# Optimization experiments

Measured on AMD Instinct MI355X. Metric: run time of the kernel, lower is better.

Reference implementation:

```python
import jax, jax.numpy as jnp
import numpy as np

B, L, E, H = 2, 2048, 2048, 16
HD = E // H  # 128
ROPE_BASE = 10000.0


def setup_inputs() -> dict:
    key = jax.random.key(0)
    k1, k2, k3 = jax.random.split(key, 3)
    x = jax.random.normal(k1, (B, L, E), dtype=jnp.float32)
    position_ids = jnp.tile(jnp.arange(L, dtype=jnp.int32)[None, :], (B, 1))
    # Linear weights stored as [in, out] so y = x @ W + b (equals torch x @ W.T + b)
    W_attn = jax.random.normal(k2, (E, 3 * E), dtype=jnp.float32) * (1.0 / np.sqrt(E))
    b_attn = jnp.zeros((3 * E,), dtype=jnp.float32)
    W_proj = jax.random.normal(k3, (E, E), dtype=jnp.float32) * (1.0 / np.sqrt(E))
    b_proj = jnp.zeros((E,), dtype=jnp.float32)
    return {"x": x, "position_ids": position_ids, "W_attn": W_attn,
            "b_attn": b_attn, "W_proj": W_proj, "b_proj": b_proj}


def _rotate_half(t):
    h = t.shape[-1] // 2
    return jnp.concatenate([-t[..., h:], t[..., :h]], axis=-1)


def _apply_rope(q, k, position_ids):
    # q,k: [B,H,L,HD]; position_ids: [B,L]
    inv_freq = 1.0 / (ROPE_BASE ** (jnp.arange(0, HD, 2, dtype=jnp.float32) / HD))
    angles = position_ids.astype(jnp.float32)[:, :, None] * inv_freq  # [B,L,HD/2]
    cos = jnp.concatenate([jnp.cos(angles)] * 2, axis=-1)[:, None]  # [B,1,L,HD]
    sin = jnp.concatenate([jnp.sin(angles)] * 2, axis=-1)[:, None]
    return q * cos + _rotate_half(q) * sin, k * cos + _rotate_half(k) * sin


def reference(x, position_ids, W_attn, b_attn, W_proj, b_proj):
    # fused QKV projection
    qkv = x @ W_attn + b_attn                       # [B,L,3E]
    q, k, v = jnp.split(qkv, 3, axis=-1)            # each [B,L,E]
    reshape = lambda t: t.reshape(B, L, H, HD).transpose(0, 2, 1, 3)  # [B,H,L,HD]
    q, k, v = reshape(q), reshape(k), reshape(v)
    q, k = _apply_rope(q, k, position_ids)
    # scaled dot-product attention (mask=None -> full attention, dropout 0)
    scores = jnp.einsum('bhqd,bhkd->bhqk', q, k) * (1.0 / np.sqrt(HD))
    probs = jax.nn.softmax(scores, axis=-1)
    y = jnp.einsum('bhqk,bhkd->bhqd', probs, v)     # [B,H,L,HD]
    y = y.transpose(0, 2, 1, 3).reshape(B, L, E)
    return y @ W_proj + b_proj
```

## Files before the change

### kernel.cpp

```cpp
#include <hip/hip_runtime.h>
#include <math.h>

#define BB 2
#define LL 2048
#define EE 2048
#define HH 16
#define HD 128
#define N3E (3*EE)

typedef __attribute__((ext_vector_type(8))) short  bf16x8;
typedef __attribute__((ext_vector_type(4))) float  f32x4;

__device__ __forceinline__ ushort f2bf(float f) {
    union { float f; unsigned u; } v; v.f = f;
    unsigned u = v.u + 0x7FFFu + ((v.u >> 16) & 1u);
    return (ushort)(u >> 16);
}
__device__ __forceinline__ float bf2f(ushort u) {
    union { unsigned u; float f; } v; v.u = ((unsigned)u) << 16;
    return v.f;
}

__global__ __launch_bounds__(256) void cvt_bf16(const float* __restrict__ in,
                                                ushort* __restrict__ out, int n) {
    int i = (blockIdx.x * 256 + threadIdx.x) * 8;
    float4 a = *(const float4*)(in + i);
    float4 b = *(const float4*)(in + i + 4);
    ushort4 p0 = { f2bf(a.x), f2bf(a.y), f2bf(a.z), f2bf(a.w) };
    ushort4 p1 = { f2bf(b.x), f2bf(b.y), f2bf(b.z), f2bf(b.w) };
    *(ushort4*)(out + i)     = p0;
    *(ushort4*)(out + i + 4) = p1;
}

__global__ __launch_bounds__(256) void transpose_bf16(const float* __restrict__ in,
                                                      ushort* __restrict__ out,
                                                      int R, int Ccol) {
    __shared__ float tile[32][33];
    int c0 = blockIdx.x * 32, r0 = blockIdx.y * 32;
    int t = threadIdx.x;
    int lr = t >> 5, lc = t & 31;
    #pragma unroll
    for (int i = 0; i < 4; ++i)
        tile[lr + i * 8][lc] = in[(size_t)(r0 + lr + i * 8) * Ccol + c0 + lc];
    __syncthreads();
    #pragma unroll
    for (int i = 0; i < 4; ++i)
        out[(size_t)(c0 + lr + i * 8) * R + r0 + lc] = f2bf(tile[lc][lr + i * 8]);
}

template<int WRITE_BF16>
__global__ __launch_bounds__(256) void gemm_bt_bf16(const ushort* __restrict__ A,
                                                    const ushort* __restrict__ Bt,
                                                    const float* __restrict__ bias,
                                                    void* __restrict__ C,
                                                    int M, int N, int K) {
    __shared__ __align__(16) ushort As[128 * 32];
    __shared__ __align__(16) ushort Bs[128 * 32];
    const int t    = threadIdx.x;
    const int lane = t & 63, w = t >> 6;
    const int m    = lane & 15, quad = lane >> 4;
    const int wm   = w >> 1, wn = w & 1;
    const int m0   = blockIdx.y * 128, n0 = blockIdx.x * 128;

    f32x4 acc[4][4];
    #pragma unroll
    for (int i = 0; i < 4; ++i)
        #pragma unroll
        for (int j = 0; j < 4; ++j) acc[i][j] = (f32x4){0.f, 0.f, 0.f, 0.f};

    for (int k0 = 0; k0 < K; k0 += 32) {
        __syncthreads();
        #pragma unroll
        for (int i = 0; i < 2; ++i) {
            int c = t + i * 256;
            int row = c >> 2, kc = c & 3;
            __builtin_amdgcn_global_load_lds(
                (const __attribute__((address_space(1))) unsigned int*)(A + (size_t)(m0 + row) * K + k0 + kc * 8),
                (__attribute__((address_space(3))) unsigned int*)(As + c * 8),
                16, 0, 0);
        }
        #pragma unroll
        for (int i = 0; i < 2; ++i) {
            int c = t + i * 256;
            int row = c >> 2, kc = c & 3;
            __builtin_amdgcn_global_load_lds(
                (const __attribute__((address_space(1))) unsigned int*)(Bt + (size_t)(n0 + row) * K + k0 + kc * 8),
                (__attribute__((address_space(3))) unsigned int*)(Bs + c * 8),
                16, 0, 0);
        }
        __syncthreads();
        bf16x8 af[4], bfr[4];
        #pragma unroll
        for (int mt = 0; mt < 4; ++mt)
            af[mt] = *(const bf16x8*)&As[(wm * 64 + mt * 16 + m) * 32 + quad * 8];
        #pragma unroll
        for (int nt = 0; nt < 4; ++nt)
            bfr[nt] = *(const bf16x8*)&Bs[(wn * 64 + nt * 16 + m) * 32 + quad * 8];
        #pragma unroll
        for (int mt = 0; mt < 4; ++mt)
            #pragma unroll
            for (int nt = 0; nt < 4; ++nt)
                acc[mt][nt] = __builtin_amdgcn_mfma_f32_16x16x32_bf16(af[mt], bfr[nt], acc[mt][nt], 0, 0, 0);
    }
    #pragma unroll
    for (int mt = 0; mt < 4; ++mt) {
        #pragma unroll
        for (int nt = 0; nt < 4; ++nt) {
            #pragma unroll
            for (int r = 0; r < 4; ++r) {
                int row = m0 + wm * 64 + mt * 16 + quad * 4 + r;
                int col = n0 + wn * 64 + nt * 16 + m;
                float v = acc[mt][nt][r] + bias[col];
                if (WRITE_BF16) ((ushort*)C)[(size_t)row * N + col] = f2bf(v);
                else            ((float*)C)[(size_t)row * N + col] = v;
            }
        }
    }
}

__global__ __launch_bounds__(256) void rope_bf16(ushort* __restrict__ qkv,
                                                 const int* __restrict__ pos_ids) {
    const float scale = 0.08838834764831845f;
    int idx = blockIdx.x * 256 + threadIdx.x;
    int j  = idx & 63;
    int h  = (idx >> 6) & 15;
    int bl = idx >> 10;
    float pos = (float)pos_ids[bl];
    float inv = powf(10000.0f, -(float)(2 * j) / 128.0f);
    float ang = pos * inv;
    float s, c;
    sincosf(ang, &s, &c);
    size_t base = (size_t)bl * N3E + h * HD;
    float x1 = bf2f(qkv[base + j]), x2 = bf2f(qkv[base + j + 64]);
    qkv[base + j]      = f2bf((x1 * c - x2 * s) * scale);
    qkv[base + j + 64] = f2bf((x2 * c + x1 * s) * scale);
    base += EE;
    x1 = bf2f(qkv[base + j]); x2 = bf2f(qkv[base + j + 64]);
    qkv[base + j]      = f2bf(x1 * c - x2 * s);
    qkv[base + j + 64] = f2bf(x2 * c + x1 * s);
}

#define BQ 64
#define BKV 64
#define QKSTR 136
#define VTSTR 72

__global__ __launch_bounds__(256) void flash_mfma(const ushort* __restrict__ qkv,
                                                  ushort* __restrict__ y) {
    __shared__ __align__(16) ushort smem[22528];
    ushort* VtU = smem;
    ushort* QsU = smem;
    ushort* KsU = smem + 9216;
    ushort* PsU = smem + 9216 + 8704;

    const int t    = threadIdx.x;
    const int w    = t >> 6;
    const int lane = t & 63;
    const int m    = lane & 15;
    const int quad = lane >> 4;
    const int q0   = blockIdx.x * BQ;
    const int bh   = blockIdx.y;
    const int b    = bh >> 4, h = bh & 15;

    const ushort* qbase = qkv + (size_t)b * LL * N3E + h * HD;
    const ushort* kbase = qbase + EE;
    const ushort* vbase = qbase + 2 * EE;

    #pragma unroll
    for (int i = 0; i < 4; ++i) {
        int idx = t + i * 256;
        int r = idx >> 4, cc = idx & 15;
        *(bf16x8*)&QsU[r * QKSTR + cc * 8] =
            *(const bf16x8*)(qbase + (size_t)(q0 + r) * N3E + cc * 8);
    }
    __syncthreads();

    bf16x8 qfrag[4];
    #pragma unroll
    for (int ks = 0; ks < 4; ++ks)
        qfrag[ks] = *(const bf16x8*)&QsU[(w * 16 + m) * QKSTR + ks * 32 + quad * 8];

    f32x4 oacc[8];
    #pragma unroll
    for (int dt = 0; dt < 8; ++dt) oacc[dt] = (f32x4){0.f, 0.f, 0.f, 0.f};
    float m_i[4], l_i[4];
    #pragma unroll
    for (int r = 0; r < 4; ++r) { m_i[r] = -INFINITY; l_i[r] = 0.f; }

    for (int kt = 0; kt < LL; kt += BKV) {
        __syncthreads();

        #pragma unroll
        for (int i = 0; i < 4; ++i) {
            int idx = t + i * 256;
            int r = idx >> 4, cc = idx & 15;
            *(bf16x8*)&KsU[r * QKSTR + cc * 8] =
                *(const bf16x8*)(kbase + (size_t)(kt + r) * N3E + cc * 8);
        }
        {
            int kb = (t >> 5) * 8;
            int dg = t & 31;
            ushort4 vv[8];
            #pragma unroll
            for (int j = 0; j < 8; ++j)
                vv[j] = *(const ushort4*)(vbase + (size_t)(kt + kb + j) * N3E + dg * 4);
            #pragma unroll
            for (int i = 0; i < 4; ++i) {
                bf16x8 pk;
                pk[0] = (short)(i == 0 ? vv[0].x : i == 1 ? vv[0].y : i == 2 ? vv[0].z : vv[0].w);
                pk[1] = (short)(i == 0 ? vv[1].x : i == 1 ? vv[1].y : i == 2 ? vv[1].z : vv[1].w);
                pk[2] = (short)(i == 0 ? vv[2].x : i == 1 ? vv[2].y : i == 2 ? vv[2].z : vv[2].w);
                pk[3] = (short)(i == 0 ? vv[3].x : i == 1 ? vv[3].y : i == 2 ? vv[3].z : vv[3].w);
                pk[4] = (short)(i == 0 ? vv[4].x : i == 1 ? vv[4].y : i == 2 ? vv[4].z : vv[4].w);
                pk[5] = (short)(i == 0 ? vv[5].x : i == 1 ? vv[5].y : i == 2 ? vv[5].z : vv[5].w);
                pk[6] = (short)(i == 0 ? vv[6].x : i == 1 ? vv[6].y : i == 2 ? vv[6].z : vv[6].w);
                pk[7] = (short)(i == 0 ? vv[7].x : i == 1 ? vv[7].y : i == 2 ? vv[7].z : vv[7].w);
                *(bf16x8*)&VtU[(dg * 4 + i) * VTSTR + kb] = pk;
            }
        }
        __syncthreads();

        f32x4 sacc[4];
        #pragma unroll
        for (int nt = 0; nt < 4; ++nt) sacc[nt] = (f32x4){0.f, 0.f, 0.f, 0.f};
        #pragma unroll
        for (int ks = 0; ks < 4; ++ks) {
            #pragma unroll
            for (int nt = 0; nt < 4; ++nt) {
                bf16x8 kf = *(const bf16x8*)&KsU[(nt * 16 + m) * QKSTR + ks * 32 + quad * 8];
                sacc[nt] = __builtin_amdgcn_mfma_f32_16x16x32_bf16(qfrag[ks], kf, sacc[nt], 0, 0, 0);
            }
        }

        float alpha[4];
        #pragma unroll
        for (int r = 0; r < 4; ++r) {
            float mx = fmaxf(fmaxf(sacc[0][r], sacc[1][r]), fmaxf(sacc[2][r], sacc[3][r]));
            #pragma unroll
            for (int off = 1; off < 16; off <<= 1) mx = fmaxf(mx, __shfl_xor(mx, off, 64));
            float mnew = fmaxf(m_i[r], mx);
            alpha[r] = __expf(m_i[r] - mnew);
            m_i[r] = mnew;
            float rs = 0.f;
            #pragma unroll
            for (int nt = 0; nt < 4; ++nt) {
                float p = __expf(sacc[nt][r] - mnew);
                sacc[nt][r] = p;
                rs += p;
            }
            #pragma unroll
            for (int off = 1; off < 16; off <<= 1) rs += __shfl_xor(rs, off, 64);
            l_i[r] = l_i[r] * alpha[r] + rs;
        }
        #pragma unroll
        for (int dt = 0; dt < 8; ++dt)
            #pragma unroll
            for (int r = 0; r < 4; ++r) oacc[dt][r] *= alpha[r];

        #pragma unroll
        for (int nt = 0; nt < 4; ++nt)
            #pragma unroll
            for (int r = 0; r < 4; ++r)
                PsU[w * 16 * VTSTR + (quad * 4 + r) * VTSTR + nt * 16 + m] = f2bf(sacc[nt][r]);

        #pragma unroll
        for (int ks2 = 0; ks2 < 2; ++ks2) {
            bf16x8 pf = *(const bf16x8*)&PsU[w * 16 * VTSTR + m * VTSTR + ks2 * 32 + quad * 8];
            #pragma unroll
            for (int dt = 0; dt < 8; ++dt) {
                bf16x8 vf = *(const bf16x8*)&VtU[(dt * 16 + m) * VTSTR + ks2 * 32 + quad * 8];
                oacc[dt] = __builtin_amdgcn_mfma_f32_16x16x32_bf16(pf, vf, oacc[dt], 0, 0, 0);
            }
        }
    }

    float linv[4];
    #pragma unroll
    for (int r = 0; r < 4; ++r) linv[r] = 1.f / l_i[r];
    #pragma unroll
    for (int dt = 0; dt < 8; ++dt) {
        #pragma unroll
        for (int r = 0; r < 4; ++r) {
            int row = q0 + w * 16 + quad * 4 + r;
            y[(size_t)(b * LL + row) * EE + h * HD + dt * 16 + m] = f2bf(oacc[dt][r] * linv[r]);
        }
    }
}

extern "C" void kernel_launch(void* const* d_in, const int* in_sizes, int n_in,
                              void* d_out, int out_size, void* d_ws, size_t ws_size,
                              hipStream_t stream) {
    const float* x      = (const float*)d_in[0];
    const int*   pos    = (const int*)d_in[1];
    const float* W_attn = (const float*)d_in[2];
    const float* b_attn = (const float*)d_in[3];
    const float* W_proj = (const float*)d_in[4];
    const float* b_proj = (const float*)d_in[5];
    float* out = (float*)d_out;

    ushort* xb   = (ushort*)d_ws;
    ushort* Wat  = xb   + (size_t)BB * LL * EE;
    ushort* Wpt  = Wat  + (size_t)N3E * EE;
    ushort* qkvb = Wpt  + (size_t)EE * EE;
    ushort* yb   = qkvb + (size_t)BB * LL * N3E;

    dim3 blk(256);
    const int M = BB * LL;

    cvt_bf16<<<dim3(M * EE / (256 * 8)), blk, 0, stream>>>(x, xb, M * EE);
    transpose_bf16<<<dim3(N3E / 32, EE / 32), blk, 0, stream>>>(W_attn, Wat, EE, N3E);
    transpose_bf16<<<dim3(EE / 32, EE / 32), blk, 0, stream>>>(W_proj, Wpt, EE, EE);

    gemm_bt_bf16<1><<<dim3(N3E / 128, M / 128), blk, 0, stream>>>(
        xb, Wat, b_attn, qkvb, M, N3E, EE);
    rope_bf16<<<dim3((BB * LL * HH * 64) / 256), blk, 0, stream>>>(qkvb, pos);
    flash_mfma<<<dim3(LL / BQ, BB * HH), blk, 0, stream>>>(qkvb, yb);
    gemm_bt_bf16<0><<<dim3(EE / 128, M / 128), blk, 0, stream>>>(
        yb, Wpt, b_proj, out, M, EE, EE);
}
```

Measured before the change: 540.2 us.

## Pre-tile swizzled Q/K/V layouts and use direct-to-LDS loads in flash attention

Replaces the in-place RoPE kernel with prep kernels that apply RoPE and write Q and K into contiguous per-head 64-row tiles with XOR-swizzled chunks, plus a pre-transposed, swizzled V tile layout. The new flash kernel fetches K/V tiles with global_load_lds straight into LDS, handles 128 query rows per block (two 16-row MFMA tiles per wave, reusing each K/V fragment), and defers the row-sum shuffle reduction to the end. This removes the strided K/V gathers and the in-kernel V transpose, at the cost of extra prep passes and buffer reuse of the workspace. Fewer, larger blocks and higher register use may reduce occupancy.

```diff
diff --git a/kernel.cpp b/kernel.cpp
--- a/kernel.cpp
+++ b/kernel.cpp
@@ -118,171 +118,213 @@
     }
 }
 
-__global__ __launch_bounds__(256) void rope_bf16(ushort* __restrict__ qkv,
-                                                 const int* __restrict__ pos_ids) {
+__global__ __launch_bounds__(256) void prep_qk(const ushort* __restrict__ qkvb,
+                                               const int* __restrict__ pos_ids,
+                                               ushort* __restrict__ Qt,
+                                               ushort* __restrict__ Kt) {
     const float scale = 0.08838834764831845f;
     int idx = blockIdx.x * 256 + threadIdx.x;
-    int j  = idx & 63;
-    int h  = (idx >> 6) & 15;
-    int bl = idx >> 10;
-    float pos = (float)pos_ids[bl];
-    float inv = powf(10000.0f, -(float)(2 * j) / 128.0f);
-    float ang = pos * inv;
-    float s, c;
-    sincosf(ang, &s, &c);
-    size_t base = (size_t)bl * N3E + h * HD;
-    float x1 = bf2f(qkv[base + j]), x2 = bf2f(qkv[base + j + 64]);
-    qkv[base + j]      = f2bf((x1 * c - x2 * s) * scale);
-    qkv[base + j + 64] = f2bf((x2 * c + x1 * s) * scale);
-    base += EE;
-    x1 = bf2f(qkv[base + j]); x2 = bf2f(qkv[base + j + 64]);
-    qkv[base + j]      = f2bf(x1 * c - x2 * s);
-    qkv[base + j + 64] = f2bf(x2 * c + x1 * s);
-}
-
-#define BQ 64
-#define BKV 64
-#define QKSTR 136
-#define VTSTR 72
-
-__global__ __launch_bounds__(256) void flash_mfma(const ushort* __restrict__ qkv,
-                                                  ushort* __restrict__ y) {
-    __shared__ __align__(16) ushort smem[22528];
-    ushort* VtU = smem;
-    ushort* QsU = smem;
-    ushort* KsU = smem + 9216;
-    ushort* PsU = smem + 9216 + 8704;
+    int p    = idx & 15;
+    int r    = (idx >> 4) & 63;
+    int tile = (idx >> 10) & 31;
+    int h    = (idx >> 15) & 15;
+    int b    = idx >> 19;
+    int c    = p ^ (r & 15);
+    int l    = tile * 64 + r;
+    int half = c >> 3, cl = c & 7;
+    const ushort* row = qkvb + (size_t)(b * LL + l) * N3E;
+    float pos = (float)pos_ids[b * LL + l];
+
+    bf16x8 qa = *(const bf16x8*)(row + h * HD + c * 8);
+    bf16x8 qb = *(const bf16x8*)(row + h * HD + (c ^ 8) * 8);
+    bf16x8 ka = *(const bf16x8*)(row + EE + h * HD + c * 8);
+    bf16x8 kb = *(const bf16x8*)(row + EE + h * HD + (c ^ 8) * 8);
+    bf16x8 qo, ko;
+    #pragma unroll
+    for (int i = 0; i < 8; ++i) {
+        int j = cl * 8 + i;
+        float ang = pos * powf(10000.0f, -(float)j / 64.0f);
+        float s, cs;
+        sincosf(ang, &s, &cs);
+        float sgn = half ? s : -s;
+        float q1 = bf2f((ushort)qa[i]), q2 = bf2f((ushort)qb[i]);
+        float k1 = bf2f((ushort)ka[i]), k2 = bf2f((ushort)kb[i]);
+        qo[i] = (short)f2bf((q1 * cs + q2 * sgn) * scale);
+        ko[i] = (short)f2bf(k1 * cs + k2 * sgn);
+    }
+    size_t obase = ((size_t)(b * 16 + h) * 32 + tile) * 8192 + r * 128 + p * 8;
+    *(bf16x8*)(Qt + obase) = qo;
+    *(bf16x8*)(Kt + obase) = ko;
+}
+
+__global__ __launch_bounds__(256) void prep_v(const ushort* __restrict__ qkvb,
+                                              ushort* __restrict__ Vtt) {
+    int idx = blockIdx.x * 256 + threadIdx.x;
+    int p    = idx & 7;
+    int r    = (idx >> 3) & 127;
+    int tile = (idx >> 10) & 31;
+    int h    = (idx >> 15) & 15;
+    int b    = idx >> 19;
+    int c    = p ^ (r & 7);
+    int col  = 2 * EE + h * HD + r;
+    bf16x8 o;
+    #pragma unroll
+    for (int i = 0; i < 8; ++i) {
+        int kk = tile * 64 + c * 8 + i;
+        o[i] = (short)qkvb[(size_t)(b * LL + kk) * N3E + col];
+    }
+    *(bf16x8*)(Vtt + ((size_t)(b * 16 + h) * 32 + tile) * 8192 + r * 64 + p * 8) = o;
+}
+
+#define PSTR 68
+
+__global__ __launch_bounds__(256, 2) void flash2(const ushort* __restrict__ Qt,
+                                                 const ushort* __restrict__ Kt,
+                                                 const ushort* __restrict__ Vtt,
+                                                 ushort* __restrict__ y) {
+    __shared__ __align__(16) ushort Ks[64 * 128];
+    __shared__ __align__(16) ushort Vs[128 * 64];
+    __shared__ __align__(16) ushort Ps[4 * 32 * PSTR];
 
     const int t    = threadIdx.x;
     const int w    = t >> 6;
     const int lane = t & 63;
     const int m    = lane & 15;
     const int quad = lane >> 4;
-    const int q0   = blockIdx.x * BQ;
+    const int qblk = blockIdx.x;
     const int bh   = blockIdx.y;
     const int b    = bh >> 4, h = bh & 15;
 
-    const ushort* qbase = qkv + (size_t)b * LL * N3E + h * HD;
-    const ushort* kbase = qbase + EE;
-    const ushort* vbase = qbase + 2 * EE;
-
-    #pragma unroll
-    for (int i = 0; i < 4; ++i) {
-        int idx = t + i * 256;
-        int r = idx >> 4, cc = idx & 15;
-        *(bf16x8*)&QsU[r * QKSTR + cc * 8] =
-            *(const bf16x8*)(qbase + (size_t)(q0 + r) * N3E + cc * 8);
-    }
-    __syncthreads();
-
-    bf16x8 qfrag[4];
-    #pragma unroll
-    for (int ks = 0; ks < 4; ++ks)
-        qfrag[ks] = *(const bf16x8*)&QsU[(w * 16 + m) * QKSTR + ks * 32 + quad * 8];
-
-    f32x4 oacc[8];
-    #pragma unroll
-    for (int dt = 0; dt < 8; ++dt) oacc[dt] = (f32x4){0.f, 0.f, 0.f, 0.f};
-    float m_i[4], l_i[4];
-    #pragma unroll
-    for (int r = 0; r < 4; ++r) { m_i[r] = -INFINITY; l_i[r] = 0.f; }
-
-    for (int kt = 0; kt < LL; kt += BKV) {
+    const ushort* Qhead = Qt  + (size_t)bh * 32 * 8192;
+    const ushort* Khead = Kt  + (size_t)bh * 32 * 8192;
+    const ushort* Vhead = Vtt + (size_t)bh * 32 * 8192;
+
+    bf16x8 qf[2][4];
+    #pragma unroll
+    for (int mt = 0; mt < 2; ++mt) {
+        int rloc = w * 32 + mt * 16 + m;
+        const ushort* qtile = Qhead + (size_t)(qblk * 2 + (rloc >> 6)) * 8192
+                              + (rloc & 63) * 128;
+        #pragma unroll
+        for (int ks = 0; ks < 4; ++ks)
+            qf[mt][ks] = *(const bf16x8*)(qtile + ((ks * 4 + quad) ^ m) * 8);
+    }
+
+    f32x4 oacc[2][8];
+    #pragma unroll
+    for (int mt = 0; mt < 2; ++mt)
+        #pragma unroll
+        for (int dt = 0; dt < 8; ++dt) oacc[mt][dt] = (f32x4){0.f, 0.f, 0.f, 0.f};
+    float m_i[8], l_pl[8];
+    #pragma unroll
+    for (int s = 0; s < 8; ++s) { m_i[s] = -INFINITY; l_pl[s] = 0.f; }
+
+    for (int kt = 0; kt < 32; ++kt) {
         __syncthreads();
-
+        const ushort* ksrc = Khead + (size_t)kt * 8192;
+        const ushort* vsrc = Vhead + (size_t)kt * 8192;
         #pragma unroll
         for (int i = 0; i < 4; ++i) {
-            int idx = t + i * 256;
-            int r = idx >> 4, cc = idx & 15;
-            *(bf16x8*)&KsU[r * QKSTR + cc * 8] =
-                *(const bf16x8*)(kbase + (size_t)(kt + r) * N3E + cc * 8);
-        }
-        {
-            int kb = (t >> 5) * 8;
-            int dg = t & 31;
-            ushort4 vv[8];
-            #pragma unroll
-            for (int j = 0; j < 8; ++j)
-                vv[j] = *(const ushort4*)(vbase + (size_t)(kt + kb + j) * N3E + dg * 4);
-            #pragma unroll
-            for (int i = 0; i < 4; ++i) {
-                bf16x8 pk;
-                pk[0] = (short)(i == 0 ? vv[0].x : i == 1 ? vv[0].y : i == 2 ? vv[0].z : vv[0].w);
-                pk[1] = (short)(i == 0 ? vv[1].x : i == 1 ? vv[1].y : i == 2 ? vv[1].z : vv[1].w);
-                pk[2] = (short)(i == 0 ? vv[2].x : i == 1 ? vv[2].y : i == 2 ? vv[2].z : vv[2].w);
-                pk[3] = (short)(i == 0 ? vv[3].x : i == 1 ? vv[3].y : i == 2 ? vv[3].z : vv[3].w);
-                pk[4] = (short)(i == 0 ? vv[4].x : i == 1 ? vv[4].y : i == 2 ? vv[4].z : vv[4].w);
-                pk[5] = (short)(i == 0 ? vv[5].x : i == 1 ? vv[5].y : i == 2 ? vv[5].z : vv[5].w);
-                pk[6] = (short)(i == 0 ? vv[6].x : i == 1 ? vv[6].y : i == 2 ? vv[6].z : vv[6].w);
-                pk[7] = (short)(i == 0 ? vv[7].x : i == 1 ? vv[7].y : i == 2 ? vv[7].z : vv[7].w);
-                *(bf16x8*)&VtU[(dg * 4 + i) * VTSTR + kb] = pk;
-            }
+            int cid = t + i * 256;
+            __builtin_amdgcn_global_load_lds(
+                (const __attribute__((address_space(1))) unsigned int*)(ksrc + cid * 8),
+                (__attribute__((address_space(3))) unsigned int*)(Ks + cid * 8),
+                16, 0, 0);
+        }
+        #pragma unroll
+        for (int i = 0; i < 4; ++i) {
+            int cid = t + i * 256;
+            __builtin_amdgcn_global_load_lds(
+                (const __attribute__((address_space(1))) unsigned int*)(vsrc + cid * 8),
+                (__attribute__((address_space(3))) unsigned int*)(Vs + cid * 8),
+                16, 0, 0);
         }
         __syncthreads();
 
-        f32x4 sacc[4];
-        #pragma unroll
-        for (int nt = 0; nt < 4; ++nt) sacc[nt] = (f32x4){0.f, 0.f, 0.f, 0.f};
+        f32x4 sacc[2][4];
+        #pragma unroll
+        for (int mt = 0; mt < 2; ++mt)
+            #pragma unroll
+            for (int nt = 0; nt < 4; ++nt) sacc[mt][nt] = (f32x4){0.f, 0.f, 0.f, 0.f};
         #pragma unroll
         for (int ks = 0; ks < 4; ++ks) {
             #pragma unroll
             for (int nt = 0; nt < 4; ++nt) {
-                bf16x8 kf = *(const bf16x8*)&KsU[(nt * 16 + m) * QKSTR + ks * 32 + quad * 8];
-                sacc[nt] = __builtin_amdgcn_mfma_f32_16x16x32_bf16(qfrag[ks], kf, sacc[nt], 0, 0, 0);
-            }
-        }
-
-        float alpha[4];
-        #pragma unroll
-        for (int r = 0; r < 4; ++r) {
-            float mx = fmaxf(fmaxf(sacc[0][r], sacc[1][r]), fmaxf(sacc[2][r], sacc[3][r]));
-            #pragma unroll
-            for (int off = 1; off < 16; off <<= 1) mx = fmaxf(mx, __shfl_xor(mx, off, 64));
-            float mnew = fmaxf(m_i[r], mx);
-            alpha[r] = __expf(m_i[r] - mnew);
-            m_i[r] = mnew;
-            float rs = 0.f;
-            #pragma unroll
-            for (int nt = 0; nt < 4; ++nt) {
-                float p = __expf(sacc[nt][r] - mnew);
-                sacc[nt][r] = p;
-                rs += p;
-            }
-            #pragma unroll
-            for (int off = 1; off < 16; off <<= 1) rs += __shfl_xor(rs, off, 64);
-            l_i[r] = l_i[r] * alpha[r] + rs;
-        }
-        #pragma unroll
-        for (int dt = 0; dt < 8; ++dt)
-            #pragma unroll
-            for (int r = 0; r < 4; ++r) oacc[dt][r] *= alpha[r];
-
-        #pragma unroll
-        for (int nt = 0; nt < 4; ++nt)
-            #pragma unroll
-            for (int r = 0; r < 4; ++r)
-                PsU[w * 16 * VTSTR + (quad * 4 + r) * VTSTR + nt * 16 + m] = f2bf(sacc[nt][r]);
+                bf16x8 kf = *(const bf16x8*)&Ks[(nt * 16 + m) * 128 + (((ks * 4 + quad) ^ m)) * 8];
+                sacc[0][nt] = __builtin_amdgcn_mfma_f32_16x16x32_bf16(qf[0][ks], kf, sacc[0][nt], 0, 0, 0);
+                sacc[1][nt] = __builtin_amdgcn_mfma_f32_16x16x32_bf16(qf[1][ks], kf, sacc[1][nt], 0, 0, 0);
+            }
+        }
+
+        float alpha_s[2][4];
+        #pragma unroll
+        for (int mt = 0; mt < 2; ++mt) {
+            #pragma unroll
+            for (int r = 0; r < 4; ++r) {
+                int slot = mt * 4 + r;
+                float mx = fmaxf(fmaxf(sacc[mt][0][r], sacc[mt][1][r]),
+                                 fmaxf(sacc[mt][2][r], sacc[mt][3][r]));
+                #pragma unroll
+                for (int off = 1; off < 16; off <<= 1) mx = fmaxf(mx, __shfl_xor(mx, off, 64));
+                float mnew = fmaxf(m_i[slot], mx);
+                float al = __expf(m_i[slot] - mnew);
+                m_i[slot] = mnew;
+                float rs = 0.f;
+                #pragma unroll
+                for (int nt = 0; nt < 4; ++nt) {
+                    float pv = __expf(sacc[mt][nt][r] - mnew);
+                    sacc[mt][nt][r] = pv;
+                    rs += pv;
+                }
+                l_pl[slot] = l_pl[slot] * al + rs;
+                alpha_s[mt][r] = al;
+            }
+        }
+        #pragma unroll
+        for (int mt = 0; mt < 2; ++mt)
+            #pragma unroll
+            for (int dt = 0; dt < 8; ++dt)
+                #pragma unroll
+                for (int r = 0; r < 4; ++r) oacc[mt][dt][r] *= alpha_s[mt][r];
+
+        #pragma unroll
+        for (int mt = 0; mt < 2; ++mt)
+            #pragma unroll
+            for (int nt = 0; nt < 4; ++nt)
+                #pragma unroll
+                for (int r = 0; r < 4; ++r)
+                    Ps[w * 32 * PSTR + (mt * 16 + quad * 4 + r) * PSTR + nt * 16 + m]
+                        = f2bf(sacc[mt][nt][r]);
 
         #pragma unroll
         for (int ks2 = 0; ks2 < 2; ++ks2) {
-            bf16x8 pf = *(const bf16x8*)&PsU[w * 16 * VTSTR + m * VTSTR + ks2 * 32 + quad * 8];
+            bf16x8 pf0 = *(const bf16x8*)&Ps[w * 32 * PSTR + (0 * 16 + m) * PSTR + ks2 * 32 + quad * 8];
+            bf16x8 pf1 = *(const bf16x8*)&Ps[w * 32 * PSTR + (1 * 16 + m) * PSTR + ks2 * 32 + quad * 8];
             #pragma unroll
             for (int dt = 0; dt < 8; ++dt) {
-                bf16x8 vf = *(const bf16x8*)&VtU[(dt * 16 + m) * VTSTR + ks2 * 32 + quad * 8];
-                oacc[dt] = __builtin_amdgcn_mfma_f32_16x16x32_bf16(pf, vf, oacc[dt], 0, 0, 0);
-            }
-        }
-    }
-
-    float linv[4];
-    #pragma unroll
-    for (int r = 0; r < 4; ++r) linv[r] = 1.f / l_i[r];
-    #pragma unroll
-    for (int dt = 0; dt < 8; ++dt) {
-        #pragma unroll
-        for (int r = 0; r < 4; ++r) {
-            int row = q0 + w * 16 + quad * 4 + r;
-            y[(size_t)(b * LL + row) * EE + h * HD + dt * 16 + m] = f2bf(oacc[dt][r] * linv[r]);
+                bf16x8 vf = *(const bf16x8*)&Vs[(dt * 16 + m) * 64 + (((ks2 * 4 + quad) ^ (m & 7))) * 8];
+                oacc[0][dt] = __builtin_amdgcn_mfma_f32_16x16x32_bf16(pf0, vf, oacc[0][dt], 0, 0, 0);
+                oacc[1][dt] = __builtin_amdgcn_mfma_f32_16x16x32_bf16(pf1, vf, oacc[1][dt], 0, 0, 0);
+            }
+        }
+    }
+
+    #pragma unroll
+    for (int s = 0; s < 8; ++s) {
+        #pragma unroll
+        for (int off = 1; off < 16; off <<= 1) l_pl[s] += __shfl_xor(l_pl[s], off, 64);
+        l_pl[s] = 1.0f / l_pl[s];
+    }
+    #pragma unroll
+    for (int mt = 0; mt < 2; ++mt) {
+        #pragma unroll
+        for (int dt = 0; dt < 8; ++dt) {
+            #pragma unroll
+            for (int r = 0; r < 4; ++r) {
+                int row = qblk * 128 + w * 32 + mt * 16 + quad * 4 + r;
+                y[(size_t)(b * LL + row) * EE + h * HD + dt * 16 + m]
+                    = f2bf(oacc[mt][dt][r] * l_pl[mt * 4 + r]);
+            }
         }
     }
 }
@@ -298,23 +340,29 @@
     const float* b_proj = (const float*)d_in[5];
     float* out = (float*)d_out;
 
+    const int M = BB * LL;
     ushort* xb   = (ushort*)d_ws;
-    ushort* Wat  = xb   + (size_t)BB * LL * EE;
+    ushort* Wat  = xb   + (size_t)M * EE;
     ushort* Wpt  = Wat  + (size_t)N3E * EE;
     ushort* qkvb = Wpt  + (size_t)EE * EE;
-    ushort* yb   = qkvb + (size_t)BB * LL * N3E;
+    ushort* Kt   = qkvb + (size_t)M * N3E;
+    ushort* Vtt  = Kt   + (size_t)M * EE;
+    ushort* Qt   = xb;
+    ushort* yb   = Wat;
 
     dim3 blk(256);
-    const int M = BB * LL;
-
     cvt_bf16<<<dim3(M * EE / (256 * 8)), blk, 0, stream>>>(x, xb, M * EE);
     transpose_bf16<<<dim3(N3E / 32, EE / 32), blk, 0, stream>>>(W_attn, Wat, EE, N3E);
     transpose_bf16<<<dim3(EE / 32, EE / 32), blk, 0, stream>>>(W_proj, Wpt, EE, EE);
 
     gemm_bt_bf16<1><<<dim3(N3E / 128, M / 128), blk, 0, stream>>>(
         xb, Wat, b_attn, qkvb, M, N3E, EE);
-    rope_bf16<<<dim3((BB * LL * HH * 64) / 256), blk, 0, stream>>>(qkvb, pos);
-    flash_mfma<<<dim3(LL / BQ, BB * HH), blk, 0, stream>>>(qkvb, yb);
+
+    prep_qk<<<dim3(4096), blk, 0, stream>>>(qkvb, pos, Qt, Kt);
+    prep_v<<<dim3(4096), blk, 0, stream>>>(qkvb, Vtt);
+
+    flash2<<<dim3(LL / 128, BB * HH), blk, 0, stream>>>(Qt, Kt, Vtt, yb);
+
     gemm_bt_bf16<0><<<dim3(EE / 128, M / 128), blk, 0, stream>>>(
         yb, Wpt, b_proj, out, M, EE, EE);
 }
```

Measured after the change: 508.5 us. -5.9%, faster.
